# Kernel tuning notes

Measured on AMD Instinct MI355X. Metric: run time of the kernel, lower is better.

## Reference

```python
import jax, jax.numpy as jnp
import numpy as np

B, T, H, NH = 4, 2048, 1024, 16
HD = H // NH  # 64


def setup_inputs() -> dict:
    key = jax.random.key(0)
    ks = jax.random.split(key, 8)
    s = 0.02
    return {
        "hidden_states": jax.random.normal(ks[0], (B, T, H), dtype=jnp.float32),
        "attention_mask": jnp.zeros((B, 1, 1, T), dtype=jnp.float32),
        "Wq": jax.random.normal(ks[1], (H, H), dtype=jnp.float32) * s,
        "bq": jnp.zeros((H,), dtype=jnp.float32),
        "Wk": jax.random.normal(ks[2], (H, H), dtype=jnp.float32) * s,
        "bk": jnp.zeros((H,), dtype=jnp.float32),
        "Wv": jax.random.normal(ks[3], (H, H), dtype=jnp.float32) * s,
        "bv": jnp.zeros((H,), dtype=jnp.float32),
    }


def _split_heads(x):
    # [B, T, H] -> [B, NH, T, HD]
    b, t, _ = x.shape
    return x.reshape(b, t, NH, HD).transpose(0, 2, 1, 3)


def reference(hidden_states, attention_mask, Wq, bq, Wk, bk, Wv, bv):
    # QKV projections (torch Linear: x @ W.T + b)
    q = _split_heads(hidden_states @ Wq.T + bq)
    k = _split_heads(hidden_states @ Wk.T + bk)
    v = _split_heads(hidden_states @ Wv.T + bv)

    scale = HD ** (-0.5)
    # [B, NH, T, T]
    scores = jnp.einsum("bhqd,bhkd->bhqk", q, k) * scale
    t = q.shape[2]
    causal = jnp.triu(jnp.ones((t, t), dtype=bool), k=1)
    scores = jnp.where(causal[None, None], -jnp.inf, scores)
    scores = scores + attention_mask  # additive mask [B,1,1,T]
    probs = jax.nn.softmax(scores, axis=-1)
    # dropout is identity in eval mode
    out = jnp.einsum("bhqk,bhkd->bhqd", probs, v)
    # [B, NH, T, HD] -> [B, T, H]
    return out.transpose(0, 2, 1, 3).reshape(hidden_states.shape[0], t, H)
```

## Files before the change

### kernel.cpp

```cpp
#include <hip/hip_runtime.h>
#include <math.h>

#define B_  4
#define T_  2048
#define H_  1024
#define NH_ 16
#define HD_ 64

typedef __bf16  bf16x8  __attribute__((ext_vector_type(8)));
typedef float   f32x4   __attribute__((ext_vector_type(4)));
typedef unsigned short ushort8v __attribute__((ext_vector_type(8)));
typedef short   short4v __attribute__((ext_vector_type(4)));

__device__ __forceinline__ unsigned short f2bf(float f) {
    unsigned int u = __builtin_bit_cast(unsigned int, f);
    u += 0x7fffu + ((u >> 16) & 1u);
    return (unsigned short)(u >> 16);
}

__device__ __forceinline__ f32x4 mfma16x16x16bf16(short4v a, short4v b, f32x4 c) {
#if __has_builtin(__builtin_amdgcn_mfma_f32_16x16x16bf16_1k)
    return __builtin_amdgcn_mfma_f32_16x16x16bf16_1k(a, b, c, 0, 0, 0);
#else
    f32x4 d = c;
    asm volatile("v_mfma_f32_16x16x16_bf16 %0, %1, %2, %0\n\ts_nop 7\n\ts_nop 7"
                 : "+v"(d) : "v"(a), "v"(b));
    return d;
#endif
}

__device__ __forceinline__ void gload_lds16(const unsigned short* g,
                                            unsigned short* l) {
    __builtin_amdgcn_global_load_lds(
        (const __attribute__((address_space(1))) unsigned int*)g,
        (__attribute__((address_space(3))) unsigned int*)l, 16, 0, 0);
}

__global__ void cvt_f32_bf16(const float* __restrict__ in,
                             unsigned short* __restrict__ out, int n8) {
    int stride = gridDim.x * blockDim.x;
    for (int i = blockIdx.x * blockDim.x + threadIdx.x; i < n8; i += stride) {
        const float4* p = reinterpret_cast<const float4*>(in) + (size_t)i * 2;
        float4 f0 = p[0], f1 = p[1];
        ushort8v o;
        o[0] = f2bf(f0.x); o[1] = f2bf(f0.y); o[2] = f2bf(f0.z); o[3] = f2bf(f0.w);
        o[4] = f2bf(f1.x); o[5] = f2bf(f1.y); o[6] = f2bf(f1.z); o[7] = f2bf(f1.w);
        reinterpret_cast<ushort8v*>(out)[i] = o;
    }
}

__global__ void cvt_w3(const float* __restrict__ Wq, const float* __restrict__ Wk,
                       const float* __restrict__ Wv,
                       unsigned short* __restrict__ oq, unsigned short* __restrict__ ok,
                       unsigned short* __restrict__ ov, int n8) {
    const int z = blockIdx.y;
    const float* in = (z == 0) ? Wq : (z == 1) ? Wk : Wv;
    unsigned short* out = (z == 0) ? oq : (z == 1) ? ok : ov;
    int stride = gridDim.x * blockDim.x;
    for (int i = blockIdx.x * blockDim.x + threadIdx.x; i < n8; i += stride) {
        const float4* p = reinterpret_cast<const float4*>(in) + (size_t)i * 2;
        float4 f0 = p[0], f1 = p[1];
        ushort8v o;
        o[0] = f2bf(f0.x); o[1] = f2bf(f0.y); o[2] = f2bf(f0.z); o[3] = f2bf(f0.w);
        o[4] = f2bf(f1.x); o[5] = f2bf(f1.y); o[6] = f2bf(f1.z); o[7] = f2bf(f1.w);
        reinterpret_cast<ushort8v*>(out)[i] = o;
    }
}

__global__ __launch_bounds__(256) void qkv_gemm_all(
    const unsigned short* __restrict__ X,
    const unsigned short* __restrict__ Wq,
    const unsigned short* __restrict__ Wk,
    const unsigned short* __restrict__ Wv,
    const float* __restrict__ bq,
    const float* __restrict__ bk,
    const float* __restrict__ bv,
    unsigned short* __restrict__ Qo,
    unsigned short* __restrict__ Ko,
    unsigned short* __restrict__ Vo)
{
    const int id     = blockIdx.x;
    const int xcd    = id & 7;
    const int within = id >> 3;
    const int z      = within >> 6;
    const int rest   = within & 63;
    const int xb     = rest >> 3;
    const int yb     = xcd * 8 + (rest & 7);

    const unsigned short* W = (z == 0) ? Wq : (z == 1) ? Wk : Wv;
    const float* bias = (z == 0) ? bq : (z == 1) ? bk : bv;
    unsigned short* out = (z == 0) ? Qo : (z == 1) ? Ko : Vo;

    const int K = 1024;
    const int t    = threadIdx.x;
    const int lane = t & 63;
    const int wid  = t >> 6;
    const int lo = lane & 15, hi = lane >> 4;
    const int wm = wid >> 1, wn = wid & 1;
    const int m0 = yb * 128;
    const int n0 = xb * 128;

    __shared__ unsigned short As[128 * 64];
    __shared__ unsigned short Bs[128 * 64];

    const int srowoff = lane >> 3;
    const int scol    = lane & 7;

    f32x4 acc[4][4];
#pragma unroll
    for (int i = 0; i < 4; ++i)
#pragma unroll
        for (int j = 0; j < 4; ++j) acc[i][j] = (f32x4){0.f, 0.f, 0.f, 0.f};

    for (int k0 = 0; k0 < K; k0 += 64) {
        __syncthreads();
#pragma unroll
        for (int p = 0; p < 4; ++p) {
            const int rowb = p * 32 + wid * 8;
            const int row  = rowb + srowoff;
            const int c16  = scol ^ (row & 7);
            gload_lds16(&X[(size_t)(m0 + row) * K + k0 + c16 * 8], &As[rowb * 64]);
            gload_lds16(&W[(size_t)(n0 + row) * K + k0 + c16 * 8], &Bs[rowb * 64]);
        }
        __syncthreads();
#pragma unroll
        for (int ks = 0; ks < 2; ++ks) {
            bf16x8 a[4], b[4];
#pragma unroll
            for (int mt = 0; mt < 4; ++mt) {
                const int row = wm * 64 + mt * 16 + lo;
                a[mt] = *reinterpret_cast<const bf16x8*>(
                    &As[row * 64 + (((ks * 4 + hi) ^ (lo & 7)) * 8)]);
            }
#pragma unroll
            for (int nt = 0; nt < 4; ++nt) {
                const int row = wn * 64 + nt * 16 + lo;
                b[nt] = *reinterpret_cast<const bf16x8*>(
                    &Bs[row * 64 + (((ks * 4 + hi) ^ (lo & 7)) * 8)]);
            }
#pragma unroll
            for (int mt = 0; mt < 4; ++mt)
#pragma unroll
                for (int nt = 0; nt < 4; ++nt)
                    acc[mt][nt] = __builtin_amdgcn_mfma_f32_16x16x32_bf16(
                        a[mt], b[nt], acc[mt][nt], 0, 0, 0);
        }
    }

#pragma unroll
    for (int nt = 0; nt < 4; ++nt) {
        int n = n0 + wn * 64 + nt * 16 + lo;
        float bv_ = bias[n];
        int h = n >> 6, d = n & 63;
#pragma unroll
        for (int mt = 0; mt < 4; ++mt) {
            int mbase = m0 + wm * 64 + mt * 16 + hi * 4;
            int bb = mbase >> 11;
            int tt = mbase & 2047;
            size_t tilebase = ((size_t)(bb * NH_ + h) * 32 + (tt >> 6)) * 4096;
            if (z == 2) {
                ushort4 pk;
                pk.x = f2bf(acc[mt][nt][0] + bv_);
                pk.y = f2bf(acc[mt][nt][1] + bv_);
                pk.z = f2bf(acc[mt][nt][2] + bv_);
                pk.w = f2bf(acc[mt][nt][3] + bv_);
                *reinterpret_cast<ushort4*>(
                    &out[tilebase + (size_t)mt * 1024 + (size_t)(hi * 16 + lo) * 16 + nt * 4]) = pk;
            } else if (z == 1) {
                const int ksd = d >> 5;
                const int hif = (d >> 3) & 3;
                const int jd  = d & 7;
                size_t fragbase = tilebase + (size_t)(mt * 2 + ksd) * 512;
#pragma unroll
                for (int r = 0; r < 4; ++r)
                    out[fragbase + (size_t)(hif * 16 + hi * 4 + r) * 8 + jd] =
                        f2bf(acc[mt][nt][r] + bv_);
            } else {
                size_t base = (size_t)(bb * NH_ + h) * T_;
#pragma unroll
                for (int r = 0; r < 4; ++r)
                    out[(base + tt + r) * HD_ + d] = f2bf(acc[mt][nt][r] + bv_);
            }
        }
    }
}

__global__ __launch_bounds__(128, 2) void attn_fwd15(
    const unsigned short* __restrict__ Q,
    const unsigned short* __restrict__ Kf,
    const unsigned short* __restrict__ Vf,
    const float* __restrict__ amask,
    float* __restrict__ out)
{
    const float SC    = 0.125f * 1.44269504089f;
    const float LOG2E = 1.44269504089f;

    const int lane = threadIdx.x & 63;
    const int w    = threadIdx.x >> 6;
    const int lo = lane & 15, hi = lane >> 4;

    const int bid    = blockIdx.x;
    const int xcd    = bid & 7;
    const int within = bid >> 3;
    const int bh     = xcd * 8 + (within & 7);
    const int u      = 63 - (within >> 3);
    const int b      = bh >> 4;
    const int h      = bh & 15;

    const unsigned short* Qg = Q + (size_t)bh * T_ * HD_;
    const float* am = amask + (size_t)b * T_;
    float* outBase = out + (size_t)b * T_ * H_ + h * HD_;

    __shared__ f32x4 Lo[2][4][64];
    __shared__ float Ll[2][64];

    const int q0   = u * 32;
    const int nt   = (u >> 1) + 1;
    const int half = nt >> 1;
    const int ktBeg = w ? half : 0;
    const int ktEnd = w ? nt : half;

    bf16x8 qf[2][2];
#pragma unroll
    for (int mt = 0; mt < 2; ++mt)
#pragma unroll
        for (int ks = 0; ks < 2; ++ks)
            qf[mt][ks] = *reinterpret_cast<const bf16x8*>(
                &Qg[(size_t)(q0 + mt * 16 + lo) * HD_ + ks * 32 + hi * 8]);

    f32x4 o[2][4];
#pragma unroll
    for (int mt = 0; mt < 2; ++mt)
#pragma unroll
        for (int dt = 0; dt < 4; ++dt) o[mt][dt] = (f32x4){0.f, 0.f, 0.f, 0.f};
    float l_r[2] = {0.f, 0.f};

    const unsigned short* kp = Kf + ((size_t)bh * 32 + ktBeg) * 4096;
    const unsigned short* vp = Vf + ((size_t)bh * 32 + ktBeg) * 4096;
    const float*          ap = am + ktBeg * 64;

    for (int kt = ktBeg; kt < ktEnd; ++kt, kp += 4096, vp += 4096, ap += 64) {
        const int kv0 = kt * 64;

        bf16x8 kf[4][2];
#pragma unroll
        for (int ct = 0; ct < 4; ++ct)
#pragma unroll
            for (int ks = 0; ks < 2; ++ks)
                kf[ct][ks] = *reinterpret_cast<const bf16x8*>(
                    &kp[(ct * 2 + ks) * 512 + lane * 8]);

        short4v vf[4][4];
#pragma unroll
        for (int ct = 0; ct < 4; ++ct) {
            union { ushort8v u8; short4v s4[2]; } va, vb;
            va.u8 = *reinterpret_cast<const ushort8v*>(&vp[ct * 1024 + lane * 16]);
            vb.u8 = *reinterpret_cast<const ushort8v*>(&vp[ct * 1024 + lane * 16 + 8]);
            vf[0][ct] = va.s4[0];
            vf[1][ct] = va.s4[1];
            vf[2][ct] = vb.s4[0];
            vf[3][ct] = vb.s4[1];
        }

        f32x4 amv[4];
#pragma unroll
        for (int ct = 0; ct < 4; ++ct)
            amv[ct] = *reinterpret_cast<const f32x4*>(&ap[ct * 16 + hi * 4]) * LOG2E;

        f32x4 s[2][4];
#pragma unroll
        for (int mt = 0; mt < 2; ++mt)
#pragma unroll
            for (int ct = 0; ct < 4; ++ct) s[mt][ct] = (f32x4){0.f, 0.f, 0.f, 0.f};
#pragma unroll
        for (int ks = 0; ks < 2; ++ks)
#pragma unroll
            for (int ct = 0; ct < 4; ++ct)
#pragma unroll
                for (int mt = 0; mt < 2; ++mt)
                    s[mt][ct] = __builtin_amdgcn_mfma_f32_16x16x32_bf16(
                        kf[ct][ks], qf[mt][ks], s[mt][ct], 0, 0, 0);

        const bool edge = (kv0 + 63 > q0);

        short4v p[2][4];
#pragma unroll
        for (int mt = 0; mt < 2; ++mt) {
            f32x4 rsv = (f32x4){0.f, 0.f, 0.f, 0.f};
#pragma unroll
            for (int ct = 0; ct < 4; ++ct) {
                f32x4 sv;
#pragma unroll
                for (int r = 0; r < 4; ++r)
                    sv[r] = fmaf(s[mt][ct][r], SC, amv[ct][r]);
                if (edge) {
                    const int q = q0 + mt * 16 + lo;
#pragma unroll
                    for (int r = 0; r < 4; ++r)
                        if (kv0 + ct * 16 + hi * 4 + r > q) sv[r] = -INFINITY;
                }
                short4v pk;
#pragma unroll
                for (int r = 0; r < 4; ++r) {
                    float pe = exp2f(sv[r]);
                    rsv[r] += pe;
                    __bf16 hb = (__bf16)pe;
                    pk[r] = __builtin_bit_cast(short, hb);
                }
                p[mt][ct] = pk;
            }
            l_r[mt] += (rsv[0] + rsv[1]) + (rsv[2] + rsv[3]);
        }

#pragma unroll
        for (int ct = 0; ct < 4; ++ct)
#pragma unroll
            for (int mt = 0; mt < 2; ++mt)
#pragma unroll
                for (int dt = 0; dt < 4; ++dt)
                    o[mt][dt] = mfma16x16x16bf16(vf[dt][ct], p[mt][ct], o[mt][dt]);
    }

    if (w == 1) {
#pragma unroll
        for (int mt = 0; mt < 2; ++mt) {
            Ll[mt][lane] = l_r[mt];
#pragma unroll
            for (int dt = 0; dt < 4; ++dt)
                Lo[mt][dt][lane] = o[mt][dt];
        }
    }
    __syncthreads();
    if (w == 0) {
#pragma unroll
        for (int mt = 0; mt < 2; ++mt) {
            float lf = l_r[mt] + Ll[mt][lane];
            lf += __shfl_xor(lf, 16, 64);
            lf += __shfl_xor(lf, 32, 64);
            const float inv = 1.0f / lf;
            const int tq = q0 + mt * 16 + lo;
            float* orow = outBase + (size_t)tq * H_;
#pragma unroll
            for (int dt = 0; dt < 4; ++dt) {
                f32x4 v = (o[mt][dt] + Lo[mt][dt][lane]) * inv;
                *reinterpret_cast<f32x4*>(&orow[dt * 16 + hi * 4]) = v;
            }
        }
    }
}

extern "C" void kernel_launch(void* const* d_in, const int* in_sizes, int n_in,
                              void* d_out, int out_size, void* d_ws, size_t ws_size,
                              hipStream_t stream) {
    const float* hs    = (const float*)d_in[0];
    const float* amask = (const float*)d_in[1];
    const float* Wq    = (const float*)d_in[2];
    const float* bq    = (const float*)d_in[3];
    const float* Wk    = (const float*)d_in[4];
    const float* bk    = (const float*)d_in[5];
    const float* Wv    = (const float*)d_in[6];
    const float* bv    = (const float*)d_in[7];
    float* out = (float*)d_out;

    unsigned short* Xbf = (unsigned short*)d_ws;
    unsigned short* Wqb = Xbf + (size_t)8192 * 1024;
    unsigned short* Wkb = Wqb + (size_t)1024 * 1024;
    unsigned short* Wvb = Wkb + (size_t)1024 * 1024;
    unsigned short* Qb  = Wvb + (size_t)1024 * 1024;
    unsigned short* Kfb = Qb  + (size_t)B_ * NH_ * T_ * HD_;
    unsigned short* Vfb = Kfb + (size_t)B_ * NH_ * T_ * HD_;

    cvt_f32_bf16<<<4096, 256, 0, stream>>>(hs, Xbf, (8192 * 1024) / 8);
    dim3 gw(512, 3);
    cvt_w3<<<gw, 256, 0, stream>>>(Wq, Wk, Wv, Wqb, Wkb, Wvb, (1024 * 1024) / 8);

    qkv_gemm_all<<<1536, 256, 0, stream>>>(Xbf, Wqb, Wkb, Wvb, bq, bk, bv,
                                           Qb, Kfb, Vfb);

    attn_fwd15<<<4096, 128, 0, stream>>>(Qb, Kfb, Vfb, amask, out);
}
```

Measured before the change: 156.8 us.

## Double-buffer LDS tiles in QKV projection GEMM to overlap loads with MFMA

The QKV projection GEMM now keeps two LDS buffers for the A and B tiles. It issues the global-to-LDS loads for the next K step before computing on the current buffer, and the K loop is fully unrolled. The goal is to hide global load latency behind MFMA work and drop one barrier per K step. In exchange it doubles LDS use to 64KB per block, which may lower occupancy, and correctness depends on the async LDS loads being complete when the barrier is reached.

```diff
diff --git a/kernel.cpp b/kernel.cpp
--- a/kernel.cpp
+++ b/kernel.cpp
@@ -100,8 +100,8 @@
     const int m0 = yb * 128;
     const int n0 = xb * 128;
 
-    __shared__ unsigned short As[128 * 64];
-    __shared__ unsigned short Bs[128 * 64];
+    __shared__ unsigned short As[2][128 * 64];
+    __shared__ unsigned short Bs[2][128 * 64];
 
     const int srowoff = lane >> 3;
     const int scol    = lane & 7;
@@ -112,39 +112,50 @@
 #pragma unroll
         for (int j = 0; j < 4; ++j) acc[i][j] = (f32x4){0.f, 0.f, 0.f, 0.f};
 
-    for (int k0 = 0; k0 < K; k0 += 64) {
+#define STAGE_(AS, BS, KOFF)                                                  \
+    do {                                                                      \
+        _Pragma("unroll") for (int p = 0; p < 4; ++p) {                       \
+            const int rowb = p * 32 + wid * 8;                                \
+            const int row  = rowb + srowoff;                                  \
+            const int c16  = scol ^ (row & 7);                                \
+            gload_lds16(&X[(size_t)(m0 + row) * K + (KOFF) + c16 * 8],        \
+                        &(AS)[rowb * 64]);                                    \
+            gload_lds16(&W[(size_t)(n0 + row) * K + (KOFF) + c16 * 8],        \
+                        &(BS)[rowb * 64]);                                    \
+        }                                                                     \
+    } while (0)
+
+#define COMPUTE_(AS, BS)                                                      \
+    do {                                                                      \
+        _Pragma("unroll") for (int ks = 0; ks < 2; ++ks) {                    \
+            bf16x8 a[4], b[4];                                                \
+            _Pragma("unroll") for (int mt = 0; mt < 4; ++mt) {                \
+                const int row = wm * 64 + mt * 16 + lo;                       \
+                a[mt] = *reinterpret_cast<const bf16x8*>(                     \
+                    &(AS)[row * 64 + (((ks * 4 + hi) ^ (lo & 7)) * 8)]);      \
+            }                                                                 \
+            _Pragma("unroll") for (int nt = 0; nt < 4; ++nt) {                \
+                const int row = wn * 64 + nt * 16 + lo;                       \
+                b[nt] = *reinterpret_cast<const bf16x8*>(                     \
+                    &(BS)[row * 64 + (((ks * 4 + hi) ^ (lo & 7)) * 8)]);      \
+            }                                                                 \
+            _Pragma("unroll") for (int mt = 0; mt < 4; ++mt)                  \
+                _Pragma("unroll") for (int nt = 0; nt < 4; ++nt)              \
+                    acc[mt][nt] = __builtin_amdgcn_mfma_f32_16x16x32_bf16(    \
+                        a[mt], b[nt], acc[mt][nt], 0, 0, 0);                  \
+        }                                                                     \
+    } while (0)
+
+    STAGE_(As[0], Bs[0], 0);
+    __syncthreads();
+#pragma unroll
+    for (int k0 = 0; k0 < K; k0 += 128) {
+        STAGE_(As[1], Bs[1], k0 + 64);
+        COMPUTE_(As[0], Bs[0]);
         __syncthreads();
-#pragma unroll
-        for (int p = 0; p < 4; ++p) {
-            const int rowb = p * 32 + wid * 8;
-            const int row  = rowb + srowoff;
-            const int c16  = scol ^ (row & 7);
-            gload_lds16(&X[(size_t)(m0 + row) * K + k0 + c16 * 8], &As[rowb * 64]);
-            gload_lds16(&W[(size_t)(n0 + row) * K + k0 + c16 * 8], &Bs[rowb * 64]);
-        }
+        if (k0 + 128 < K) STAGE_(As[0], Bs[0], k0 + 128);
+        COMPUTE_(As[1], Bs[1]);
         __syncthreads();
-#pragma unroll
-        for (int ks = 0; ks < 2; ++ks) {
-            bf16x8 a[4], b[4];
-#pragma unroll
-            for (int mt = 0; mt < 4; ++mt) {
-                const int row = wm * 64 + mt * 16 + lo;
-                a[mt] = *reinterpret_cast<const bf16x8*>(
-                    &As[row * 64 + (((ks * 4 + hi) ^ (lo & 7)) * 8)]);
-            }
-#pragma unroll
-            for (int nt = 0; nt < 4; ++nt) {
-                const int row = wn * 64 + nt * 16 + lo;
-                b[nt] = *reinterpret_cast<const bf16x8*>(
-                    &Bs[row * 64 + (((ks * 4 + hi) ^ (lo & 7)) * 8)]);
-            }
-#pragma unroll
-            for (int mt = 0; mt < 4; ++mt)
-#pragma unroll
-                for (int nt = 0; nt < 4; ++nt)
-                    acc[mt][nt] = __builtin_amdgcn_mfma_f32_16x16x32_bf16(
-                        a[mt], b[nt], acc[mt][nt], 0, 0, 0);
-        }
     }
 
 #pragma unroll
@@ -183,6 +194,8 @@
             }
         }
     }
+#undef STAGE_
+#undef COMPUTE_
 }
 
 __global__ __launch_bounds__(128, 2) void attn_fwd15(
```

New measurement: 154.3 us. Within noise of the previous version (-1.6%).
